# Optimization experiments

Hardware: AMD Instinct MI355X
Metric: run time of the kernel (lower is better)

Reference implementation:

```python
import jax, jax.numpy as jnp
import numpy as np

NUM_LAYERS = 24
LN_EPS = 1e-5


def setup_inputs() -> dict:
    key = jax.random.key(0)
    ks = jax.random.split(key, 8)
    B, S = 256, 8192
    x = jax.random.uniform(ks[0], (B, S, 5), dtype=jnp.float32)
    # per-layer LayerNorm(4) params (torch default init: weight=1, bias=0; use
    # randomized values so the gather is non-trivial)
    ln_w = 1.0 + 0.1 * jax.random.normal(ks[1], (NUM_LAYERS, 4), dtype=jnp.float32)
    ln_b = 0.1 * jax.random.normal(ks[2], (NUM_LAYERS, 4), dtype=jnp.float32)
    # MLP 5 -> 64 -> 32 -> 1 (dropout inactive in eval mode)
    W1 = jax.random.normal(ks[3], (64, 5), dtype=jnp.float32) / np.sqrt(5)
    b1 = jnp.zeros((64,), dtype=jnp.float32)
    W2 = jax.random.normal(ks[4], (32, 64), dtype=jnp.float32) / np.sqrt(64)
    b2 = jnp.zeros((32,), dtype=jnp.float32)
    W3 = jax.random.normal(ks[5], (1, 32), dtype=jnp.float32) / np.sqrt(32)
    b3 = jnp.zeros((1,), dtype=jnp.float32)
    return {"x": x, "ln_w": ln_w, "ln_b": ln_b, "W1": W1, "b1": b1,
            "W2": W2, "b2": b2, "W3": W3, "b3": b3}


def reference(x, ln_w, ln_b, W1, b1, W2, b2, W3, b3):
    B, S, _ = x.shape
    x_flat = x.reshape(-1, 5)                      # [N, 5]
    layer_pos = x_flat[:, -1]                      # [N]
    layer_ids = jnp.clip((layer_pos * NUM_LAYERS).astype(jnp.int32), 0, NUM_LAYERS - 1)
    feats = x_flat[:, :4]                          # [N, 4]
    # vectorized per-token LayerNorm: gather per-token gamma/beta by layer id
    mean = jnp.mean(feats, axis=-1, keepdims=True)
    var = jnp.mean(jnp.square(feats - mean), axis=-1, keepdims=True)  # biased, as torch LN
    normed = (feats - mean) * jax.lax.rsqrt(var + LN_EPS)
    normed = normed * ln_w[layer_ids] + ln_b[layer_ids]               # [N, 4]
    x_norm = jnp.concatenate([normed, layer_pos[:, None]], axis=1)    # [N, 5]
    h = jax.nn.relu(x_norm @ W1.T + b1)            # [N, 64]
    h = jax.nn.relu(h @ W2.T + b2)                 # [N, 32]
    scores = h @ W3.T + b3                         # [N, 1]
    return scores.reshape(B, S)
```

## Files before the change

### kernel.cpp

```cpp
#include <hip/hip_runtime.h>
#include <stdint.h>

#define NUM_LAYERS 24
#define LN_EPS 1e-5f
#define N_ROWS (256 * 8192)
#define ROWS_PER_ITER 64
#define NUM_ITERS (N_ROWS / ROWS_PER_ITER)
#define NUM_BLOCKS 2048

typedef __attribute__((ext_vector_type(4)))  uint32_t u32x4;
typedef __attribute__((ext_vector_type(16))) float    f32x16;
typedef __attribute__((ext_vector_type(2)))  float    f32x2;
typedef __attribute__((ext_vector_type(2)))  __fp16   h16x2;

__device__ __forceinline__ uint32_t pk_f16_rtz(float lo, float hi) {
    h16x2 v = __builtin_amdgcn_cvt_pkrtz(lo, hi);
    uint32_t u; __builtin_memcpy(&u, &v, 4);
    return u;
}
__device__ __forceinline__ uint32_t pk_f16_rne(float lo, float hi) {
    __fp16 a = (__fp16)lo, b = (__fp16)hi;
    uint16_t ua, ub;
    __builtin_memcpy(&ua, &a, 2); __builtin_memcpy(&ub, &b, 2);
    return (uint32_t)ua | ((uint32_t)ub << 16);
}
__device__ __forceinline__ uint32_t pk_relu_f16(uint32_t d) {
    h16x2 v; __builtin_memcpy(&v, &d, 4);
    h16x2 z = {(__fp16)0.0f, (__fp16)0.0f};
    v = __builtin_elementwise_max(v, z);
    uint32_t u; __builtin_memcpy(&u, &v, 4);
    return u;
}

__device__ __forceinline__ u32x4 make_frag(uint32_t d0, uint32_t d1,
                                           uint32_t d2, uint32_t d3) {
    u32x4 f; f.x = d0; f.y = d1; f.z = d2; f.w = d3;
    return f;
}

__device__ __forceinline__ void mfma_l1(f32x16& d0, f32x16& d1,
                                        f32x16& d2, f32x16& d3,
                                        const u32x4& a0, const u32x4& a1,
                                        const u32x4& b0, const u32x4& b1) {
    asm("s_nop 2\n\t"
        "v_mfma_f32_32x32x16_f16 %0, %4, %6, 0\n\t"
        "v_mfma_f32_32x32x16_f16 %1, %5, %6, 0\n\t"
        "v_mfma_f32_32x32x16_f16 %2, %4, %7, 0\n\t"
        "v_mfma_f32_32x32x16_f16 %3, %5, %7, 0"
        : "=&v"(d0), "=&v"(d1), "=&v"(d2), "=&v"(d3)
        : "v"(a0), "v"(a1), "v"(b0), "v"(b1));
}
__device__ __forceinline__ void mfma_l2(f32x16& c0, f32x16& c1, const f32x16& cinit,
                                        const u32x4& w0, const u32x4& w1,
                                        const u32x4& w2, const u32x4& w3,
                                        const u32x4& h00, const u32x4& h01,
                                        const u32x4& h02, const u32x4& h03,
                                        const u32x4& h10, const u32x4& h11,
                                        const u32x4& h12, const u32x4& h13) {
    asm("s_nop 2\n\t"
        "v_mfma_f32_32x32x16_f16 %0, %3, %7, %2\n\t"
        "v_mfma_f32_32x32x16_f16 %1, %3, %11, %2\n\t"
        "v_mfma_f32_32x32x16_f16 %0, %4, %8, %0\n\t"
        "v_mfma_f32_32x32x16_f16 %1, %4, %12, %1\n\t"
        "v_mfma_f32_32x32x16_f16 %0, %5, %9, %0\n\t"
        "v_mfma_f32_32x32x16_f16 %1, %5, %13, %1\n\t"
        "v_mfma_f32_32x32x16_f16 %0, %6, %10, %0\n\t"
        "v_mfma_f32_32x32x16_f16 %1, %6, %14, %1"
        : "=&v"(c0), "=&v"(c1)
        : "v"(cinit), "v"(w0), "v"(w1), "v"(w2), "v"(w3),
          "v"(h00), "v"(h01), "v"(h02), "v"(h03),
          "v"(h10), "v"(h11), "v"(h12), "v"(h13));
}
__device__ __forceinline__ void mfma_fence2(f32x16& c0, f32x16& c1) {
    asm volatile("s_nop 7\n\ts_nop 7\n\ts_nop 7" : "+v"(c0), "+v"(c1));
}
__device__ __forceinline__ void mfma_fence4(f32x16& c0, f32x16& c1,
                                            f32x16& c2, f32x16& c3) {
    asm volatile("s_nop 7\n\ts_nop 7\n\ts_nop 7"
                 : "+v"(c0), "+v"(c1), "+v"(c2), "+v"(c3));
}

__device__ __forceinline__ int sigma_k(int p) {
    int hh = (p >> 2) & 1;
    int base = (p & 31) - 4 * hh;
    int r = (base & 3) + 4 * (base >> 3);
    return 32 * (p >> 5) + 16 * (r >> 3) + 8 * hh + (r & 7);
}

__global__ __launch_bounds__(256, 3) void router_mfma(
    const float* __restrict__ x,
    const float* __restrict__ ln_w,
    const float* __restrict__ ln_b,
    const float* __restrict__ W1,
    const float* __restrict__ b1,
    const float* __restrict__ W2,
    const float* __restrict__ b2,
    const float* __restrict__ W3,
    const float* __restrict__ b3,
    float* __restrict__ out)
{
    __shared__ float s_ln[8 * NUM_LAYERS];
    __shared__ float s_x[4][ROWS_PER_ITER * 5];

    const int t = threadIdx.x;
    if (t < 8 * NUM_LAYERS) {
        const int q = t & 7, lid = t >> 3;
        s_ln[q * NUM_LAYERS + lid] =
            (q < 4) ? ln_w[lid * 4 + q] : ln_b[lid * 4 + (q - 4)];
    }
    __syncthreads();

    const int lane = t & 63;
    const int wid  = t >> 6;
    const int n32  = lane & 31;
    const int h    = lane >> 5;

    u32x4 a1f[2];
#pragma unroll
    for (int mt = 0; mt < 2; ++mt) {
        int p = mt * 32 + n32;
        int k = sigma_k(p);
        uint32_t d0 = pk_f16_rne(W1[k * 5 + 0], W1[k * 5 + 1]);
        uint32_t d1 = pk_f16_rne(W1[k * 5 + 2], W1[k * 5 + 3]);
        uint32_t d2 = pk_f16_rne(W1[k * 5 + 4], b1[k]);
        if (h) { d0 = 0; d1 = 0; d2 = 0; }
        a1f[mt] = make_frag(d0, d1, d2, 0);
    }

    u32x4 w2f[4];
#pragma unroll
    for (int kt = 0; kt < 4; ++kt) {
        const float* wp = W2 + n32 * 64 + kt * 16 + h * 8;
        const float4 lo = *(const float4*)(wp);
        const float4 hi = *(const float4*)(wp + 4);
        w2f[kt] = make_frag(pk_f16_rne(lo.x, lo.y), pk_f16_rne(lo.z, lo.w),
                            pk_f16_rne(hi.x, hi.y), pk_f16_rne(hi.z, hi.w));
    }

    f32x16 c2init;
    f32x2 w3p[8];
#pragma unroll
    for (int r2 = 0; r2 < 8; ++r2) {
        const int n = ((2 * r2) & 3) + 8 * (r2 >> 1) + 4 * h;
        w3p[r2] = f32x2{W3[n], W3[n + 1]};
        c2init[2 * r2]     = b2[n];
        c2init[2 * r2 + 1] = b2[n + 1];
    }
    const float b3v = b3[0];
    const f32x2 z2 = {0.0f, 0.0f};

    const int total_waves = NUM_BLOCKS * 4;
    const int w = blockIdx.x * 4 + wid;

    float* const sx = &s_x[wid][0];
    const float* const sxr = sx + 5 * lane;

    int it = w;
    {
        const float* xg = x + (size_t)it * (ROWS_PER_ITER * 5);
        float ld[5];
#pragma unroll
        for (int j = 0; j < 5; ++j) ld[j] = xg[j * 64 + lane];
#pragma unroll
        for (int j = 0; j < 5; ++j) sx[j * 64 + lane] = ld[j];
    }
    float f0 = sxr[0], f1 = sxr[1], f2 = sxr[2], f3 = sxr[3], lp = sxr[4];

    while (true) {
        const int nit = it + total_waves;
        const bool more = nit < NUM_ITERS;
        const float* xg = x + (size_t)(more ? nit : it) * (ROWS_PER_ITER * 5);
        float ld[5];
#pragma unroll
        for (int j = 0; j < 5; ++j) ld[j] = xg[j * 64 + lane];

        const int rowBase = it * ROWS_PER_ITER;

        int lid = (int)(lp * (float)NUM_LAYERS);
        lid = lid < 0 ? 0 : (lid > NUM_LAYERS - 1 ? NUM_LAYERS - 1 : lid);

        const float m  = (f0 + f1 + f2 + f3) * 0.25f;
        const float d0 = f0 - m, d1 = f1 - m, d2 = f2 - m, d3 = f3 - m;
        const float var = (d0 * d0 + d1 * d1 + d2 * d2 + d3 * d3) * 0.25f;
#if __has_builtin(__builtin_amdgcn_rsqf)
        const float r = __builtin_amdgcn_rsqf(var + LN_EPS);
#else
        const float r = rsqrtf(var + LN_EPS);
#endif
        const float rg0 = r * s_ln[0 * 24 + lid];
        const float rg1 = r * s_ln[1 * 24 + lid];
        const float rg2 = r * s_ln[2 * 24 + lid];
        const float rg3 = r * s_ln[3 * 24 + lid];
        const float xn0 = fmaf(d0, rg0, s_ln[4 * 24 + lid]);
        const float xn1 = fmaf(d1, rg1, s_ln[5 * 24 + lid]);
        const float xn2 = fmaf(d2, rg2, s_ln[6 * 24 + lid]);
        const float xn3 = fmaf(d3, rg3, s_ln[7 * 24 + lid]);

        const uint32_t e0 = pk_f16_rtz(xn0, xn1);
        const uint32_t e1 = pk_f16_rtz(xn2, xn3);
        const uint32_t e2 = pk_f16_rtz(lp, 1.0f);
        const uint32_t x0 = __shfl_xor((int)e0, 32, 64);
        const uint32_t x1 = __shfl_xor((int)e1, 32, 64);
        const uint32_t x2 = __shfl_xor((int)e2, 32, 64);

        const u32x4 bf_t0 = make_frag(e0, e1, e2, 0u);
        const u32x4 bf_t1 = make_frag(x0, x1, x2, 0u);

        f32x16 c1a0, c1b0, c1a1, c1b1;
        mfma_l1(c1a0, c1b0, c1a1, c1b1, a1f[0], a1f[1], bf_t0, bf_t1);
        mfma_fence4(c1a0, c1b0, c1a1, c1b1);

        u32x4 h1f0[4], h1f1[4];
#pragma unroll
        for (int kt = 0; kt < 4; ++kt) {
            const f32x16& c1 = (kt < 2) ? c1a0 : c1b0;
            const int roff = 8 * (kt & 1);
            uint32_t dw[4];
#pragma unroll
            for (int d = 0; d < 4; ++d)
                dw[d] = pk_relu_f16(
                    pk_f16_rtz(c1[roff + 2 * d], c1[roff + 2 * d + 1]));
            h1f0[kt] = make_frag(dw[0], dw[1], dw[2], dw[3]);
        }
#pragma unroll
        for (int kt = 0; kt < 4; ++kt) {
            const f32x16& c1 = (kt < 2) ? c1a1 : c1b1;
            const int roff = 8 * (kt & 1);
            uint32_t dw[4];
#pragma unroll
            for (int d = 0; d < 4; ++d)
                dw[d] = pk_relu_f16(
                    pk_f16_rtz(c1[roff + 2 * d], c1[roff + 2 * d + 1]));
            h1f1[kt] = make_frag(dw[0], dw[1], dw[2], dw[3]);
        }

        f32x16 c2_0, c2_1;
        mfma_l2(c2_0, c2_1, c2init,
                w2f[0], w2f[1], w2f[2], w2f[3],
                h1f0[0], h1f0[1], h1f0[2], h1f0[3],
                h1f1[0], h1f1[1], h1f1[2], h1f1[3]);
        mfma_fence2(c2_0, c2_1);

        f32x2 acc0 = z2, acc1 = z2;
#pragma unroll
        for (int r2 = 0; r2 < 8; ++r2) {
            f32x2 v0 = {c2_0[2 * r2], c2_0[2 * r2 + 1]};
            f32x2 v1 = {c2_1[2 * r2], c2_1[2 * r2 + 1]};
            v0 = __builtin_elementwise_max(v0, z2);
            v1 = __builtin_elementwise_max(v1, z2);
            acc0 = v0 * w3p[r2] + acc0;
            acc1 = v1 * w3p[r2] + acc1;
        }
        float p0 = acc0.x + acc0.y;
        float p1 = acc1.x + acc1.y;
        p0 += __shfl_xor(p0, 32, 64);
        p1 += __shfl_xor(p1, 32, 64);

        out[rowBase + lane] = (h ? p1 : p0) + b3v;

#pragma unroll
        for (int j = 0; j < 5; ++j) sx[j * 64 + lane] = ld[j];
        f0 = sxr[0]; f1 = sxr[1]; f2 = sxr[2]; f3 = sxr[3]; lp = sxr[4];

        if (!more) break;
        it = nit;
    }
}

extern "C" void kernel_launch(void* const* d_in, const int* in_sizes, int n_in,
                              void* d_out, int out_size, void* d_ws, size_t ws_size,
                              hipStream_t stream) {
    const float* x    = (const float*)d_in[0];
    const float* ln_w = (const float*)d_in[1];
    const float* ln_b = (const float*)d_in[2];
    const float* W1   = (const float*)d_in[3];
    const float* b1   = (const float*)d_in[4];
    const float* W2   = (const float*)d_in[5];
    const float* b2   = (const float*)d_in[6];
    const float* W3   = (const float*)d_in[7];
    const float* b3   = (const float*)d_in[8];
    float* out = (float*)d_out;

    router_mfma<<<NUM_BLOCKS, 256, 0, stream>>>(x, ln_w, ln_b, W1, b1, W2, b2,
                                                W3, b3, out);
}
```

Baseline: 108.3 us.

## Load rows directly with float4 and process two 64-row groups per iteration

Removes the LDS transpose staging buffer: each lane now loads its own row as an unaligned float4 plus a scalar straight from global memory, instead of coalesced strided loads followed by a shared-memory round trip. Each wave iteration now covers 128 rows in two groups, with the next iteration's loads prefetched into registers. This saves LDS traffic and synchronization-free shared writes and reads, but the per-lane 20-byte stride gives less coalesced and misaligned vector loads, and register pressure rises.

```diff
diff --git a/kernel.cpp b/kernel.cpp
--- a/kernel.cpp
+++ b/kernel.cpp
@@ -4,7 +4,7 @@
 #define NUM_LAYERS 24
 #define LN_EPS 1e-5f
 #define N_ROWS (256 * 8192)
-#define ROWS_PER_ITER 64
+#define ROWS_PER_ITER 128
 #define NUM_ITERS (N_ROWS / ROWS_PER_ITER)
 #define NUM_BLOCKS 2048
 
@@ -100,7 +100,6 @@
     float* __restrict__ out)
 {
     __shared__ float s_ln[8 * NUM_LAYERS];
-    __shared__ float s_x[4][ROWS_PER_ITER * 5];
 
     const int t = threadIdx.x;
     if (t < 8 * NUM_LAYERS) {
@@ -152,118 +151,111 @@
     const int total_waves = NUM_BLOCKS * 4;
     const int w = blockIdx.x * 4 + wid;
 
-    float* const sx = &s_x[wid][0];
-    const float* const sxr = sx + 5 * lane;
-
     int it = w;
     {
-        const float* xg = x + (size_t)it * (ROWS_PER_ITER * 5);
-        float ld[5];
-#pragma unroll
-        for (int j = 0; j < 5; ++j) ld[j] = xg[j * 64 + lane];
-#pragma unroll
-        for (int j = 0; j < 5; ++j) sx[j * 64 + lane] = ld[j];
-    }
-    float f0 = sxr[0], f1 = sxr[1], f2 = sxr[2], f3 = sxr[3], lp = sxr[4];
-
-    while (true) {
-        const int nit = it + total_waves;
-        const bool more = nit < NUM_ITERS;
-        const float* xg = x + (size_t)(more ? nit : it) * (ROWS_PER_ITER * 5);
-        float ld[5];
-#pragma unroll
-        for (int j = 0; j < 5; ++j) ld[j] = xg[j * 64 + lane];
-
-        const int rowBase = it * ROWS_PER_ITER;
-
-        int lid = (int)(lp * (float)NUM_LAYERS);
-        lid = lid < 0 ? 0 : (lid > NUM_LAYERS - 1 ? NUM_LAYERS - 1 : lid);
-
-        const float m  = (f0 + f1 + f2 + f3) * 0.25f;
-        const float d0 = f0 - m, d1 = f1 - m, d2 = f2 - m, d3 = f3 - m;
-        const float var = (d0 * d0 + d1 * d1 + d2 * d2 + d3 * d3) * 0.25f;
-#if __has_builtin(__builtin_amdgcn_rsqf)
-        const float r = __builtin_amdgcn_rsqf(var + LN_EPS);
-#else
-        const float r = rsqrtf(var + LN_EPS);
-#endif
-        const float rg0 = r * s_ln[0 * 24 + lid];
-        const float rg1 = r * s_ln[1 * 24 + lid];
-        const float rg2 = r * s_ln[2 * 24 + lid];
-        const float rg3 = r * s_ln[3 * 24 + lid];
-        const float xn0 = fmaf(d0, rg0, s_ln[4 * 24 + lid]);
-        const float xn1 = fmaf(d1, rg1, s_ln[5 * 24 + lid]);
-        const float xn2 = fmaf(d2, rg2, s_ln[6 * 24 + lid]);
-        const float xn3 = fmaf(d3, rg3, s_ln[7 * 24 + lid]);
-
-        const uint32_t e0 = pk_f16_rtz(xn0, xn1);
-        const uint32_t e1 = pk_f16_rtz(xn2, xn3);
-        const uint32_t e2 = pk_f16_rtz(lp, 1.0f);
-        const uint32_t x0 = __shfl_xor((int)e0, 32, 64);
-        const uint32_t x1 = __shfl_xor((int)e1, 32, 64);
-        const uint32_t x2 = __shfl_xor((int)e2, 32, 64);
-
-        const u32x4 bf_t0 = make_frag(e0, e1, e2, 0u);
-        const u32x4 bf_t1 = make_frag(x0, x1, x2, 0u);
-
-        f32x16 c1a0, c1b0, c1a1, c1b1;
-        mfma_l1(c1a0, c1b0, c1a1, c1b1, a1f[0], a1f[1], bf_t0, bf_t1);
-        mfma_fence4(c1a0, c1b0, c1a1, c1b1);
-
-        u32x4 h1f0[4], h1f1[4];
-#pragma unroll
-        for (int kt = 0; kt < 4; ++kt) {
-            const f32x16& c1 = (kt < 2) ? c1a0 : c1b0;
-            const int roff = 8 * (kt & 1);
-            uint32_t dw[4];
-#pragma unroll
-            for (int d = 0; d < 4; ++d)
-                dw[d] = pk_relu_f16(
-                    pk_f16_rtz(c1[roff + 2 * d], c1[roff + 2 * d + 1]));
-            h1f0[kt] = make_frag(dw[0], dw[1], dw[2], dw[3]);
+        const float* p0 = x + (size_t)(it * ROWS_PER_ITER + lane) * 5;
+        const float* p1 = x + (size_t)(it * ROWS_PER_ITER + 64 + lane) * 5;
+        float4 c40 = *(const float4*)p0; float cl0 = p0[4];
+        float4 c41 = *(const float4*)p1; float cl1 = p1[4];
+
+        while (true) {
+            const int nit = it + total_waves;
+            const bool more = nit < NUM_ITERS;
+            const size_t nb = (size_t)(more ? nit : it) * ROWS_PER_ITER;
+            const float* n0 = x + (nb + lane) * 5;
+            const float* n1 = x + (nb + 64 + lane) * 5;
+            const float4 nv40 = *(const float4*)n0; const float nl0 = n0[4];
+            const float4 nv41 = *(const float4*)n1; const float nl1 = n1[4];
+
+            const int rowBase = it * ROWS_PER_ITER;
+
+#pragma unroll
+            for (int grp = 0; grp < 2; ++grp) {
+                const float4 cv = grp ? c41 : c40;
+                const float  cl = grp ? cl1 : cl0;
+                const int gbase = rowBase + 64 * grp;
+
+                int lid = (int)(cl * (float)NUM_LAYERS);
+                lid = lid < 0 ? 0 : (lid > NUM_LAYERS - 1 ? NUM_LAYERS - 1 : lid);
+
+                const float m  = (cv.x + cv.y + cv.z + cv.w) * 0.25f;
+                const float d0 = cv.x - m, d1 = cv.y - m,
+                            d2 = cv.z - m, d3 = cv.w - m;
+                const float var = (d0 * d0 + d1 * d1 + d2 * d2 + d3 * d3) * 0.25f;
+                const float r   = rsqrtf(var + LN_EPS);
+
+                const float xn0 = fmaf(d0, r * s_ln[0 * 24 + lid], s_ln[4 * 24 + lid]);
+                const float xn1 = fmaf(d1, r * s_ln[1 * 24 + lid], s_ln[5 * 24 + lid]);
+                const float xn2 = fmaf(d2, r * s_ln[2 * 24 + lid], s_ln[6 * 24 + lid]);
+                const float xn3 = fmaf(d3, r * s_ln[3 * 24 + lid], s_ln[7 * 24 + lid]);
+
+                const uint32_t e0 = pk_f16_rtz(xn0, xn1);
+                const uint32_t e1 = pk_f16_rtz(xn2, xn3);
+                const uint32_t e2 = pk_f16_rtz(cl, 1.0f);
+                const uint32_t x0 = __shfl_xor((int)e0, 32, 64);
+                const uint32_t x1 = __shfl_xor((int)e1, 32, 64);
+                const uint32_t x2 = __shfl_xor((int)e2, 32, 64);
+
+                const u32x4 bf_t0 = make_frag(e0, e1, e2, 0u);
+                const u32x4 bf_t1 = make_frag(x0, x1, x2, 0u);
+
+                f32x16 c1a0, c1b0, c1a1, c1b1;
+                mfma_l1(c1a0, c1b0, c1a1, c1b1, a1f[0], a1f[1], bf_t0, bf_t1);
+                mfma_fence4(c1a0, c1b0, c1a1, c1b1);
+
+                u32x4 h1f0[4], h1f1[4];
+#pragma unroll
+                for (int kt = 0; kt < 4; ++kt) {
+                    const f32x16& c1 = (kt < 2) ? c1a0 : c1b0;
+                    const int roff = 8 * (kt & 1);
+                    uint32_t dw[4];
+#pragma unroll
+                    for (int d = 0; d < 4; ++d)
+                        dw[d] = pk_relu_f16(
+                            pk_f16_rtz(c1[roff + 2 * d], c1[roff + 2 * d + 1]));
+                    h1f0[kt] = make_frag(dw[0], dw[1], dw[2], dw[3]);
+                }
+#pragma unroll
+                for (int kt = 0; kt < 4; ++kt) {
+                    const f32x16& c1 = (kt < 2) ? c1a1 : c1b1;
+                    const int roff = 8 * (kt & 1);
+                    uint32_t dw[4];
+#pragma unroll
+                    for (int d = 0; d < 4; ++d)
+                        dw[d] = pk_relu_f16(
+                            pk_f16_rtz(c1[roff + 2 * d], c1[roff + 2 * d + 1]));
+                    h1f1[kt] = make_frag(dw[0], dw[1], dw[2], dw[3]);
+                }
+
+                f32x16 c2_0, c2_1;
+                mfma_l2(c2_0, c2_1, c2init,
+                        w2f[0], w2f[1], w2f[2], w2f[3],
+                        h1f0[0], h1f0[1], h1f0[2], h1f0[3],
+                        h1f1[0], h1f1[1], h1f1[2], h1f1[3]);
+                mfma_fence2(c2_0, c2_1);
+
+                f32x2 acc0 = z2, acc1 = z2;
+#pragma unroll
+                for (int r2 = 0; r2 < 8; ++r2) {
+                    f32x2 v0 = {c2_0[2 * r2], c2_0[2 * r2 + 1]};
+                    f32x2 v1 = {c2_1[2 * r2], c2_1[2 * r2 + 1]};
+                    v0 = __builtin_elementwise_max(v0, z2);
+                    v1 = __builtin_elementwise_max(v1, z2);
+                    acc0 = v0 * w3p[r2] + acc0;
+                    acc1 = v1 * w3p[r2] + acc1;
+                }
+                float q0 = acc0.x + acc0.y;
+                float q1 = acc1.x + acc1.y;
+                q0 += __shfl_xor(q0, 32, 64);
+                q1 += __shfl_xor(q1, 32, 64);
+
+                out[gbase + lane] = (h ? q1 : q0) + b3v;
+            }
+
+            if (!more) break;
+            it = nit;
+            c40 = nv40; cl0 = nl0; c41 = nv41; cl1 = nl1;
         }
-#pragma unroll
-        for (int kt = 0; kt < 4; ++kt) {
-            const f32x16& c1 = (kt < 2) ? c1a1 : c1b1;
-            const int roff = 8 * (kt & 1);
-            uint32_t dw[4];
-#pragma unroll
-            for (int d = 0; d < 4; ++d)
-                dw[d] = pk_relu_f16(
-                    pk_f16_rtz(c1[roff + 2 * d], c1[roff + 2 * d + 1]));
-            h1f1[kt] = make_frag(dw[0], dw[1], dw[2], dw[3]);
-        }
-
-        f32x16 c2_0, c2_1;
-        mfma_l2(c2_0, c2_1, c2init,
-                w2f[0], w2f[1], w2f[2], w2f[3],
-                h1f0[0], h1f0[1], h1f0[2], h1f0[3],
-                h1f1[0], h1f1[1], h1f1[2], h1f1[3]);
-        mfma_fence2(c2_0, c2_1);
-
-        f32x2 acc0 = z2, acc1 = z2;
-#pragma unroll
-        for (int r2 = 0; r2 < 8; ++r2) {
-            f32x2 v0 = {c2_0[2 * r2], c2_0[2 * r2 + 1]};
-            f32x2 v1 = {c2_1[2 * r2], c2_1[2 * r2 + 1]};
-            v0 = __builtin_elementwise_max(v0, z2);
-            v1 = __builtin_elementwise_max(v1, z2);
-            acc0 = v0 * w3p[r2] + acc0;
-            acc1 = v1 * w3p[r2] + acc1;
-        }
-        float p0 = acc0.x + acc0.y;
-        float p1 = acc1.x + acc1.y;
-        p0 += __shfl_xor(p0, 32, 64);
-        p1 += __shfl_xor(p1, 32, 64);
-
-        out[rowBase + lane] = (h ? p1 : p0) + b3v;
-
-#pragma unroll
-        for (int j = 0; j < 5; ++j) sx[j * 64 + lane] = ld[j];
-        f0 = sxr[0]; f1 = sxr[1]; f2 = sxr[2]; f3 = sxr[3]; lp = sxr[4];
-
-        if (!more) break;
-        it = nit;
     }
 }
 
```

Result: no change. 108.2 us (-0.1%).
